# Optimization experiments

Measured on AMD Instinct MI355X. Metric: run time of the kernel, lower is better.

Reference implementation:

```python
import jax, jax.numpy as jnp
import numpy as np

N, B = 128, 8                                # seq_len, batch
V, E, H, S, T = 32000, 256, 256, 256, 32     # vocab, embed, hidden, segment_dim, segment_threshold


def _gru_cell(x, h, Wi, Wh, bi, bh):
    # PyTorch GRU cell convention (gates ordered r,z,n)
    gi = x @ Wi.T + bi
    gh = h @ Wh.T + bh
    ir, iz, inn = jnp.split(gi, 3, axis=-1)
    hr, hz, hn = jnp.split(gh, 3, axis=-1)
    r = jax.nn.sigmoid(ir + hr)
    z = jax.nn.sigmoid(iz + hz)
    n = jnp.tanh(inn + r * hn)
    return (1.0 - z) * n + z * h


def _run_gru(xs, h0, Wi, Wh, bi, bh):
    def step(h, x):
        h = _gru_cell(x, h, Wi, Wh, bi, bh)
        return h, h
    hT, ys = jax.lax.scan(step, h0, xs)
    return ys, hT


def setup_inputs() -> dict:
    key = jax.random.key(0)
    ks = jax.random.split(key, 17)
    sc = 1.0 / np.sqrt(H).astype(np.float32)
    w = lambda k, shape: jax.random.normal(k, shape, jnp.float32) * sc
    return {
        "tokens": jax.random.randint(ks[0], (N, B), 0, V, dtype=jnp.int32),
        "emb": w(ks[1], (V, E)),
        "Wi_f": w(ks[2], (3 * H, E)), "Wh_f": w(ks[3], (3 * H, H)),
        "bi_f": w(ks[4], (3 * H,)),  "bh_f": w(ks[5], (3 * H,)),
        "Wi_r": w(ks[6], (3 * H, E)), "Wh_r": w(ks[7], (3 * H, H)),
        "bi_r": w(ks[8], (3 * H,)),  "bh_r": w(ks[9], (3 * H,)),
        "Wi_s": w(ks[10], (3 * S, 2 * H)), "Wh_s": w(ks[11], (3 * S, S)),
        "bi_s": w(ks[12], (3 * S,)), "bh_s": w(ks[13], (3 * S,)),
        # deterministic stand-ins for the per-start torch.randn initial hiddens
        "h0f": jax.random.normal(ks[14], (N, B, S), jnp.float32),
        "h0b": jax.random.normal(ks[15], (N, B, S), jnp.float32),
    }


def reference(tokens, emb, Wi_f, Wh_f, bi_f, bh_f, Wi_r, Wh_r, bi_r, bh_r,
              Wi_s, Wh_s, bi_s, bh_s, h0f, h0b):
    x = emb[tokens]                                   # (N,B,E); dropout p=0
    h0 = jnp.zeros((B, H), x.dtype)
    ys_f, _ = _run_gru(x, h0, Wi_f, Wh_f, bi_f, bh_f)
    ys_r, _ = _run_gru(x[::-1], h0, Wi_r, Wh_r, bi_r, bh_r)
    outputs = jnp.concatenate([ys_f, ys_r[::-1]], axis=-1)   # (N,B,2H)

    def seg(window, h0i):                             # window (T,B,2H)
        def step(h, xt):
            h = _gru_cell(xt, h, Wi_s, Wh_s, bi_s, bh_s)
            return h, h
        hT, ys = jax.lax.scan(step, h0i, window)
        return ys, hT

    ii = jnp.arange(N)[:, None]                       # (N,1) segment start i
    tt = jnp.arange(T)[None, :]                       # (1,T) step within window
    jf = ii + tt                                      # forward target column j
    jb = ii - tt                                      # backward target row j
    win_f = outputs[jnp.clip(jf, 0, N - 1)]           # (N,T,B,2H)
    win_b = outputs[jnp.clip(jb, 0, N - 1)]
    outs_f, _ = jax.vmap(seg)(win_f, h0f)             # (N,T,B,S)
    outs_b, hT_b = jax.vmap(seg)(win_b, h0b)

    jf_s = jnp.where(jf < N, jf, N)                   # OOB index -> dropped
    jb_s = jnp.where(jb >= 0, jb, N)
    dp_f = jnp.zeros((N, N, B, S), outputs.dtype).at[ii, jf_s].set(outs_f, mode="drop")
    dp_b = jnp.zeros((N, N, B, S), outputs.dtype).at[jb_s, ii].set(outs_b, mode="drop")
    dp = jnp.concatenate([dp_f, dp_b], axis=-1)       # (N,N,B,2S)
    rows, cols = jnp.triu_indices(N)
    dp_tri = dp[rows, cols]                           # (N*(N+1)/2, B, 2S)

    # final hiddens as the torch loops leave them: forward i=N-1 runs exactly
    # one step; backward i=N-1 runs T steps (N >= T so all in range).
    hid_f = _gru_cell(outputs[-1], h0f[-1], Wi_s, Wh_s, bi_s, bh_s)
    hidden = jnp.concatenate([hid_f, hT_b[-1]], axis=-1)[None]  # (1,B,2S)
    return dp_tri, hidden
```

## Files before the change

kernel.cpp:

```cpp
#include <hip/hip_runtime.h>
#include <cstdint>
#include <cstddef>

#define NN 128
#define BB 8
#define EE 256
#define HH 256
#define SS 256
#define TT 32
#define G3 768
#define HBSTR 264
#define HIDOFF 33816576ull
#define OUT_ELEMS 33820672ull

typedef __attribute__((ext_vector_type(8))) short bf16x8;
typedef __attribute__((ext_vector_type(4))) float f32x4;
typedef _Float16 f16;
typedef __attribute__((ext_vector_type(2))) _Float16 f16x2;

__device__ __forceinline__ float bf2f(unsigned short u) {
    union { unsigned u; float f; } v; v.u = ((unsigned)u) << 16; return v.f;
}
__device__ __forceinline__ unsigned short f2bf(float f) {
    union { float f; unsigned u; } v; v.f = f;
    unsigned r = v.u + 0x7fffu + ((v.u >> 16) & 1u);
    return (unsigned short)(r >> 16);
}
__device__ __forceinline__ unsigned short f2h(float f) {
    union { f16 h; unsigned short u; } v; v.h = (f16)f; return v.u;
}
__device__ __forceinline__ float dot2h(unsigned wu, unsigned hu, float acc) {
    union { unsigned u; f16x2 h; } a, b2;
    a.u = wu; b2.u = hu;
    return __builtin_amdgcn_fdot2(a.h, b2.h, acc, false);
}
__device__ __forceinline__ float rcpf(float x) { return __builtin_amdgcn_rcpf(x); }
__device__ __forceinline__ float sigm(float x) { return rcpf(1.f + __expf(-x)); }
__device__ __forceinline__ float tanh_fast(float x) {
    float xc = fminf(fmaxf(x, -10.f), 10.f);
    float e2 = __expf(2.f * xc);
    return (e2 - 1.f) * rcpf(e2 + 1.f);
}

__device__ __forceinline__ int detect_f32(const void* emb) {
    const unsigned* w = (const unsigned*)emb;
    int bad = 0;
    for (int i = 0; i < 128; ++i) {
        unsigned u = w[i];
        bad |= (((u >> 7)  & 0xFFu) >= 0xC8u);
        bad |= (((u >> 23) & 0xFFu) >= 0xC8u);
    }
    return bad;
}
__device__ __forceinline__ float lds1(const void* p, size_t i, int f32) {
    return f32 ? ((const float*)p)[i] : bf2f(((const unsigned short*)p)[i]);
}
__device__ __forceinline__ void outw(void* p, size_t i, float v, int f32) {
    if (f32) ((float*)p)[i] = v;
    else ((unsigned short*)p)[i] = f2bf(v);
}

__global__ __launch_bounds__(256) void conv_all(
    const void* __restrict__ Wi_f, const void* __restrict__ Wi_r,
    const void* __restrict__ Wh_f, const void* __restrict__ Wh_r,
    const void* __restrict__ Wh_s, const void* __restrict__ Wi_s,
    unsigned short* __restrict__ dst, const void* __restrict__ emb) {
    const int f32 = detect_f32(emb);
    size_t i = ((size_t)blockIdx.x * 256 + threadIdx.x) * 8;
    const void* src; size_t off; int h16 = 0;
    if      (i < 196608)  { src = Wi_f; off = i; }
    else if (i < 393216)  { src = Wi_r; off = i - 196608; }
    else if (i < 589824)  { src = Wh_f; off = i - 393216; h16 = 1; }
    else if (i < 786432)  { src = Wh_r; off = i - 589824; h16 = 1; }
    else if (i < 983040)  { src = Wh_s; off = i - 786432; }
    else                  { src = Wi_s; off = i - 983040; }
    bf16x8 v;
    if (f32) {
        const float* q = (const float*)src + off;
        float4 a = *(const float4*)q, b4 = *(const float4*)(q + 4);
        float f[8] = {a.x, a.y, a.z, a.w, b4.x, b4.y, b4.z, b4.w};
#pragma unroll
        for (int j = 0; j < 8; ++j)
            v[j] = (short)(h16 ? f2h(f[j]) : f2bf(f[j]));
    } else {
        v = *(const bf16x8*)((const unsigned short*)src + off);
        if (h16) {
#pragma unroll
            for (int j = 0; j < 8; ++j)
                v[j] = (short)f2h(bf2f((unsigned short)v[j]));
        }
    }
    *(bf16x8*)(dst + i) = v;
}

template <int KK>
__global__ __launch_bounds__(256) void gemm_mfma(
    const int* __restrict__ tok, const void* __restrict__ Asrc,
    const unsigned short* __restrict__ W,  const void* __restrict__ bias,
    unsigned short* __restrict__ C,
    const unsigned short* __restrict__ W2, const void* __restrict__ bias2,
    unsigned short* __restrict__ C2, const void* __restrict__ emb) {

    const int f32 = detect_f32(emb);
    __shared__ unsigned short As[64 * 260];

    int bid = blockIdx.x;
    const unsigned short* Wp = W; const void* bp = bias; unsigned short* Cp = C;
    if (C2 && bid >= 128) { bid -= 128; Wp = W2; bp = bias2; Cp = C2; }
    const int mb = bid >> 3, nb = bid & 7;

    const int tid = threadIdx.x, wave = tid >> 6, lane = tid & 63;
    const int l15 = lane & 15, quad = lane >> 4;

    f32x4 acc[6];
#pragma unroll
    for (int nt = 0; nt < 6; ++nt) acc[nt] = (f32x4){0.f, 0.f, 0.f, 0.f};

    for (int kh = 0; kh < KK; kh += 256) {
        __syncthreads();
        for (int e = tid * 4; e < 64 * 256; e += 1024) {
            int r = e >> 8, k = e & 255;
            int gr = mb * 64 + r;
            unsigned short h4[4];
            if (tok) {
                size_t arow = (size_t)tok[gr] * EE + kh + k;
                if (f32) {
                    float4 v = *(const float4*)((const float*)Asrc + arow);
                    h4[0] = f2bf(v.x); h4[1] = f2bf(v.y); h4[2] = f2bf(v.z); h4[3] = f2bf(v.w);
                } else {
                    *(uint2*)h4 = *(const uint2*)((const unsigned short*)Asrc + arow);
                }
            } else {
                *(uint2*)h4 = *(const uint2*)((const unsigned short*)Asrc + (size_t)gr * KK + kh + k);
            }
            *(uint2*)(As + r * 260 + k) = *(uint2*)h4;
        }
        __syncthreads();
#pragma unroll
        for (int kt = 0; kt < 8; ++kt) {
            bf16x8 Af = *(const bf16x8*)(As + (wave * 16 + l15) * 260 + kt * 32 + quad * 8);
#pragma unroll
            for (int nt = 0; nt < 6; ++nt) {
                int col = nb * 96 + nt * 16 + l15;
                bf16x8 Bfr = *(const bf16x8*)(Wp + (size_t)col * KK + kh + kt * 32 + quad * 8);
                acc[nt] = __builtin_amdgcn_mfma_f32_16x16x32_bf16(Af, Bfr, acc[nt], 0, 0, 0);
            }
        }
    }
#pragma unroll
    for (int nt = 0; nt < 6; ++nt) {
        int col = nb * 96 + nt * 16 + l15;
        float bv = lds1(bp, col, f32);
#pragma unroll
        for (int r4 = 0; r4 < 4; ++r4) {
            int row = mb * 64 + wave * 16 + quad * 4 + r4;
            Cp[(size_t)row * G3 + col] = f2bf(acc[nt][r4] + bv);
        }
    }
}

__global__ __attribute__((amdgpu_flat_work_group_size(512, 512), amdgpu_waves_per_eu(2, 2)))
void token_scan_zero(
    const unsigned short* __restrict__ gi_f, const unsigned short* __restrict__ gi_r,
    const unsigned short* __restrict__ Wh_fh, const unsigned short* __restrict__ Wh_rh,
    const void* __restrict__ bh_f, const void* __restrict__ bh_r,
    unsigned short* __restrict__ outp, void* __restrict__ dout,
    const void* __restrict__ emb) {

    const int f32 = detect_f32(emb);

    if (blockIdx.x >= 16) {
        uint4 z = {0u, 0u, 0u, 0u};
        uint4* p = (uint4*)dout;
        const size_t nvec = OUT_ELEMS * (f32 ? 4 : 2) / 16;
        size_t stride = (size_t)(gridDim.x - 16) * 512;
        for (size_t v = (size_t)(blockIdx.x - 16) * 512 + threadIdx.x; v < nvec; v += stride)
            p[v] = z;
        return;
    }

    const int dir = blockIdx.x & 1;
    const int b   = blockIdx.x >> 1;
    const int tid = threadIdx.x;
    const int c = tid & 255, kh = tid >> 8;

    __shared__ __align__(16) unsigned short hbs[256];
    __shared__ float pr[3][256];

    const unsigned short* Wh = dir ? Wh_rh : Wh_fh;
    const unsigned short* gi = dir ? gi_r : gi_f;
    const void* bh = dir ? bh_r : bh_f;

    unsigned w[192];
#pragma unroll
    for (int g = 0; g < 3; ++g) {
        const unsigned* wp = (const unsigned*)(Wh + (size_t)(g * 256 + c) * 256 + kh * 128);
#pragma unroll
        for (int q = 0; q < 16; ++q) {
            uint4 v = *(const uint4*)(wp + q * 4);
            w[g * 64 + q * 4 + 0] = v.x; w[g * 64 + q * 4 + 1] = v.y;
            w[g * 64 + q * 4 + 2] = v.z; w[g * 64 + q * 4 + 3] = v.w;
        }
    }
#pragma unroll
    for (int i = 0; i < 192; ++i) asm volatile("" : "+v"(w[i]));

    const float bh0 = lds1(bh, c, f32);
    const float bh1 = lds1(bh, c + 256, f32);
    const float bh2 = lds1(bh, c + 512, f32);

    if (tid < 256) hbs[tid] = 0;
    float hreg = 0.f;
    __syncthreads();

    const unsigned* hbw = (const unsigned*)hbs + kh * 64;
    for (int t = 0; t < NN; ++t) {
        const int row = dir ? (NN - 1 - t) : t;
        unsigned short g0 = 0, g1 = 0, g2 = 0;
        if (kh == 0) {
            const unsigned short* gp = gi + (size_t)row * BB * G3 + (size_t)b * G3;
            g0 = gp[c]; g1 = gp[c + 256]; g2 = gp[c + 512];
        }
        float a0 = 0.f, a1 = 0.f, a2 = 0.f;
#pragma unroll
        for (int q = 0; q < 16; ++q) {
            uint4 hv = *(const uint4*)(hbw + q * 4);
            a0 = dot2h(w[      q * 4 + 0], hv.x, a0);
            a0 = dot2h(w[      q * 4 + 1], hv.y, a0);
            a0 = dot2h(w[      q * 4 + 2], hv.z, a0);
            a0 = dot2h(w[      q * 4 + 3], hv.w, a0);
            a1 = dot2h(w[ 64 + q * 4 + 0], hv.x, a1);
            a1 = dot2h(w[ 64 + q * 4 + 1], hv.y, a1);
            a1 = dot2h(w[ 64 + q * 4 + 2], hv.z, a1);
            a1 = dot2h(w[ 64 + q * 4 + 3], hv.w, a1);
            a2 = dot2h(w[128 + q * 4 + 0], hv.x, a2);
            a2 = dot2h(w[128 + q * 4 + 1], hv.y, a2);
            a2 = dot2h(w[128 + q * 4 + 2], hv.z, a2);
            a2 = dot2h(w[128 + q * 4 + 3], hv.w, a2);
        }
        if (kh) { pr[0][c] = a0; pr[1][c] = a1; pr[2][c] = a2; }
        __syncthreads();
        if (kh == 0) {
            a0 += pr[0][c]; a1 += pr[1][c]; a2 += pr[2][c];
            float rr = sigm(bf2f(g0) + a0 + bh0);
            float zz = sigm(bf2f(g1) + a1 + bh1);
            float nn = tanh_fast(bf2f(g2) + rr * (a2 + bh2));
            float hn = (1.f - zz) * nn + zz * hreg;
            hreg = hn;
            hbs[c] = f2h(hn);
        }
        __syncthreads();
        if (kh == 0)
            outp[((size_t)(row * BB + b)) * 512 + dir * 256 + c] = f2bf(hreg);
    }
}

__global__ __attribute__((amdgpu_flat_work_group_size(512, 512), amdgpu_waves_per_eu(2, 2)))
void seg_scan(
    const unsigned short* __restrict__ gi,
    const unsigned short* __restrict__ Whc,
    const void* __restrict__ bh,
    const void* __restrict__ h0f, const void* __restrict__ h0b,
    void* __restrict__ dout, const void* __restrict__ emb) {

    const int f32 = detect_f32(emb);

    __shared__ float gh[BB][G3];
    __shared__ __align__(16) unsigned short hb[16 * HBSTR];

    const int tid = threadIdx.x;
    const int wave = tid >> 6, lane = tid & 63;
    const int l15 = lane & 15, quad = lane >> 4;
    const int dir = blockIdx.x & 1, i0 = blockIdx.x >> 1;

    bf16x8 Ba[8][6];
#pragma unroll
    for (int nt = 0; nt < 6; ++nt) {
        int col = wave * 96 + nt * 16 + l15;
#pragma unroll
        for (int kt = 0; kt < 8; ++kt)
            Ba[kt][nt] = *(const bf16x8*)(Whc + (size_t)col * 256 + kt * 32 + quad * 8);
    }
#pragma unroll
    for (int kt = 0; kt < 8; ++kt)
#pragma unroll
        for (int nt = 0; nt < 6; ++nt) asm volatile("" : "+a"(Ba[kt][nt]));

    const void* h0 = dir ? h0b : h0f;
    const size_t h0base = (size_t)i0 * (BB * SS);
    const int c = tid & 255;
    const int half = tid >> 8;
    const float bh0 = lds1(bh, c, f32);
    const float bh1 = lds1(bh, c + 256, f32);
    const float bh2 = lds1(bh, c + 512, f32);
    float hreg[4];
#pragma unroll
    for (int q = 0; q < 4; ++q) {
        int b = half * 4 + q;
        float v = lds1(h0, h0base + b * 256 + c, f32);
        hreg[q] = v;
        hb[b * HBSTR + c] = f2bf(v);
    }
    for (int e = 8 * HBSTR + tid; e < 16 * HBSTR; e += 512) hb[e] = 0;
    __syncthreads();

    const int nsteps = dir ? min(TT, i0 + 1) : min(TT, NN - i0);
    for (int t = 0; t < nsteps; ++t) {
        const int j = dir ? (i0 - t) : (i0 + t);
        unsigned short gpre[4][3];
        const unsigned short* gp = gi + (size_t)j * BB * G3;
#pragma unroll
        for (int q = 0; q < 4; ++q) {
            int b = half * 4 + q;
            gpre[q][0] = gp[b * G3 + c];
            gpre[q][1] = gp[b * G3 + c + 256];
            gpre[q][2] = gp[b * G3 + c + 512];
        }
        {
            f32x4 acc[6];
#pragma unroll
            for (int nt = 0; nt < 6; ++nt) acc[nt] = (f32x4){0.f, 0.f, 0.f, 0.f};
#pragma unroll
            for (int kt = 0; kt < 8; ++kt) {
                bf16x8 Af = *(const bf16x8*)(hb + l15 * HBSTR + kt * 32 + quad * 8);
#pragma unroll
                for (int nt = 0; nt < 6; ++nt)
                    acc[nt] = __builtin_amdgcn_mfma_f32_16x16x32_bf16(Af, Ba[kt][nt], acc[nt], 0, 0, 0);
            }
            if (quad < 2) {
#pragma unroll
                for (int nt = 0; nt < 6; ++nt) {
                    int col = wave * 96 + nt * 16 + l15;
#pragma unroll
                    for (int r4 = 0; r4 < 4; ++r4) gh[quad * 4 + r4][col] = acc[nt][r4];
                }
            }
        }
        __syncthreads();

#pragma unroll
        for (int q = 0; q < 4; ++q) {
            int b = half * 4 + q;
            float rr = sigm(bf2f(gpre[q][0]) + gh[b][c] + bh0);
            float zz = sigm(bf2f(gpre[q][1]) + gh[b][c + 256] + bh1);
            float nn = tanh_fast(bf2f(gpre[q][2]) + rr * (gh[b][c + 512] + bh2));
            float hn = (1.f - zz) * nn + zz * hreg[q];
            hreg[q] = hn;
            hb[b * HBSTR + c] = f2bf(hn);
        }
        __syncthreads();

        const int r0 = dir ? j : i0;
        const size_t tri = (size_t)r0 * NN - (size_t)(r0 * (r0 - 1)) / 2 + t;
        const size_t obase = tri * (BB * 512) + (dir ? 256 : 0);
#pragma unroll
        for (int q = 0; q < 4; ++q) {
            int b = half * 4 + q;
            outw(dout, obase + b * 512 + c, hreg[q], f32);
            if (i0 == NN - 1) {
                if (dir == 0 && t == 0)      outw(dout, HIDOFF + b * 512 + c, hreg[q], f32);
                if (dir == 1 && t == TT - 1) outw(dout, HIDOFF + 256 + b * 512 + c, hreg[q], f32);
            }
        }
    }
}

extern "C" void kernel_launch(void* const* d_in, const int* in_sizes, int n_in,
                              void* d_out, int out_size, void* d_ws, size_t ws_size,
                              hipStream_t stream) {
    const int* tokens = (const int*)d_in[0];
    const void* emb   = d_in[1];
    const void* Wi_f  = d_in[2];
    const void* Wh_f  = d_in[3];
    const void* bi_f  = d_in[4];
    const void* bh_f  = d_in[5];
    const void* Wi_r  = d_in[6];
    const void* Wh_r  = d_in[7];
    const void* bi_r  = d_in[8];
    const void* bh_r  = d_in[9];
    const void* Wi_s  = d_in[10];
    const void* Wh_s  = d_in[11];
    const void* bi_s  = d_in[12];
    const void* bh_s  = d_in[13];
    const void* h0f   = d_in[14];
    const void* h0b   = d_in[15];

    unsigned short* wsu = (unsigned short*)d_ws;
    unsigned short* gif  = wsu;
    unsigned short* gir  = wsu + 786432;
    unsigned short* outp = wsu + 1572864;
    unsigned short* wcv  = wsu + 2097152;
    unsigned short* gis  = gif;

    const unsigned short* Wi_fc = wcv;
    const unsigned short* Wi_rc = wcv + 196608;
    const unsigned short* Wh_fh = wcv + 393216;
    const unsigned short* Wh_rh = wcv + 589824;
    const unsigned short* Wh_sc = wcv + 786432;
    const unsigned short* Wi_sc = wcv + 983040;

    conv_all<<<dim3(672), dim3(256), 0, stream>>>(Wi_f, Wi_r, Wh_f, Wh_r, Wh_s, Wi_s,
                                                  wcv, emb);
    gemm_mfma<256><<<dim3(256), dim3(256), 0, stream>>>(
        tokens, emb, Wi_fc, bi_f, gif, Wi_rc, bi_r, gir, emb);
    token_scan_zero<<<dim3(256), dim3(512), 0, stream>>>(gif, gir, Wh_fh, Wh_rh,
                                                         bh_f, bh_r, outp, d_out, emb);
    gemm_mfma<512><<<dim3(128), dim3(256), 0, stream>>>(
        nullptr, outp, Wi_sc, bi_s, gis, nullptr, nullptr, nullptr, emb);
    seg_scan<<<dim3(256), dim3(512), 0, stream>>>(gis, Wh_sc, bh_s, h0f, h0b, d_out, emb);
}
```

Baseline: 539.0 us.

## Halve seg_scan block to 4 waves holding 12 weight tiles each; nontemporal zero stores

seg_scan now runs with 256 threads (4 waves) instead of 512. Each wave keeps 12 MFMA column tiles of the recurrent weight, split between AGPRs and VGPRs, and each thread handles all 8 batch elements in the elementwise GRU update. This raises per-wave MFMA work but halves the waves that synchronize at each barrier, and it targets one wave per EU, so latency hiding is lower and register pressure is high. Separately, the output-zeroing loop uses nontemporal stores to avoid polluting the cache.

```diff
diff --git a/kernel.cpp b/kernel.cpp
--- a/kernel.cpp
+++ b/kernel.cpp
@@ -15,6 +15,7 @@
 
 typedef __attribute__((ext_vector_type(8))) short bf16x8;
 typedef __attribute__((ext_vector_type(4))) float f32x4;
+typedef __attribute__((ext_vector_type(4))) unsigned u32x4;
 typedef _Float16 f16;
 typedef __attribute__((ext_vector_type(2))) _Float16 f16x2;
 
@@ -170,12 +171,12 @@
     const int f32 = detect_f32(emb);
 
     if (blockIdx.x >= 16) {
-        uint4 z = {0u, 0u, 0u, 0u};
-        uint4* p = (uint4*)dout;
+        u32x4 z = (u32x4){0u, 0u, 0u, 0u};
+        u32x4* p = (u32x4*)dout;
         const size_t nvec = OUT_ELEMS * (f32 ? 4 : 2) / 16;
         size_t stride = (size_t)(gridDim.x - 16) * 512;
         for (size_t v = (size_t)(blockIdx.x - 16) * 512 + threadIdx.x; v < nvec; v += stride)
-            p[v] = z;
+            __builtin_nontemporal_store(z, p + v);
         return;
     }
 
@@ -255,7 +256,7 @@
     }
 }
 
-__global__ __attribute__((amdgpu_flat_work_group_size(512, 512), amdgpu_waves_per_eu(2, 2)))
+__global__ __attribute__((amdgpu_flat_work_group_size(256, 256), amdgpu_waves_per_eu(1, 1)))
 void seg_scan(
     const unsigned short* __restrict__ gi,
     const unsigned short* __restrict__ Whc,
@@ -273,64 +274,69 @@
     const int l15 = lane & 15, quad = lane >> 4;
     const int dir = blockIdx.x & 1, i0 = blockIdx.x >> 1;
 
-    bf16x8 Ba[8][6];
-#pragma unroll
-    for (int nt = 0; nt < 6; ++nt) {
-        int col = wave * 96 + nt * 16 + l15;
-#pragma unroll
-        for (int kt = 0; kt < 8; ++kt)
-            Ba[kt][nt] = *(const bf16x8*)(Whc + (size_t)col * 256 + kt * 32 + quad * 8);
-    }
-#pragma unroll
-    for (int kt = 0; kt < 8; ++kt)
-#pragma unroll
-        for (int nt = 0; nt < 6; ++nt) asm volatile("" : "+a"(Ba[kt][nt]));
+    bf16x8 Ba[8][8]; bf16x8 Bv[8][4];
+#pragma unroll
+    for (int nt = 0; nt < 12; ++nt) {
+        int col = wave * 192 + nt * 16 + l15;
+#pragma unroll
+        for (int kt = 0; kt < 8; ++kt) {
+            bf16x8 f = *(const bf16x8*)(Whc + (size_t)col * 256 + kt * 32 + quad * 8);
+            if (nt < 8) Ba[kt][nt] = f; else Bv[kt][nt - 8] = f;
+        }
+    }
+#pragma unroll
+    for (int kt = 0; kt < 8; ++kt) {
+#pragma unroll
+        for (int nt = 0; nt < 8; ++nt) asm volatile("" : "+a"(Ba[kt][nt]));
+#pragma unroll
+        for (int nt = 0; nt < 4; ++nt) asm volatile("" : "+v"(Bv[kt][nt]));
+    }
 
     const void* h0 = dir ? h0b : h0f;
     const size_t h0base = (size_t)i0 * (BB * SS);
-    const int c = tid & 255;
-    const int half = tid >> 8;
+    const int c = tid;
     const float bh0 = lds1(bh, c, f32);
     const float bh1 = lds1(bh, c + 256, f32);
     const float bh2 = lds1(bh, c + 512, f32);
-    float hreg[4];
-#pragma unroll
-    for (int q = 0; q < 4; ++q) {
-        int b = half * 4 + q;
+    float hreg[BB];
+#pragma unroll
+    for (int b = 0; b < BB; ++b) {
         float v = lds1(h0, h0base + b * 256 + c, f32);
-        hreg[q] = v;
+        hreg[b] = v;
         hb[b * HBSTR + c] = f2bf(v);
     }
-    for (int e = 8 * HBSTR + tid; e < 16 * HBSTR; e += 512) hb[e] = 0;
+    for (int e = 8 * HBSTR + tid; e < 16 * HBSTR; e += 256) hb[e] = 0;
     __syncthreads();
 
     const int nsteps = dir ? min(TT, i0 + 1) : min(TT, NN - i0);
     for (int t = 0; t < nsteps; ++t) {
         const int j = dir ? (i0 - t) : (i0 + t);
-        unsigned short gpre[4][3];
+        unsigned short gpre[BB][3];
         const unsigned short* gp = gi + (size_t)j * BB * G3;
 #pragma unroll
-        for (int q = 0; q < 4; ++q) {
-            int b = half * 4 + q;
-            gpre[q][0] = gp[b * G3 + c];
-            gpre[q][1] = gp[b * G3 + c + 256];
-            gpre[q][2] = gp[b * G3 + c + 512];
+        for (int b = 0; b < BB; ++b) {
+            gpre[b][0] = gp[b * G3 + c];
+            gpre[b][1] = gp[b * G3 + c + 256];
+            gpre[b][2] = gp[b * G3 + c + 512];
         }
         {
-            f32x4 acc[6];
-#pragma unroll
-            for (int nt = 0; nt < 6; ++nt) acc[nt] = (f32x4){0.f, 0.f, 0.f, 0.f};
+            f32x4 acc[12];
+#pragma unroll
+            for (int nt = 0; nt < 12; ++nt) acc[nt] = (f32x4){0.f, 0.f, 0.f, 0.f};
 #pragma unroll
             for (int kt = 0; kt < 8; ++kt) {
                 bf16x8 Af = *(const bf16x8*)(hb + l15 * HBSTR + kt * 32 + quad * 8);
 #pragma unroll
-                for (int nt = 0; nt < 6; ++nt)
+                for (int nt = 0; nt < 8; ++nt)
                     acc[nt] = __builtin_amdgcn_mfma_f32_16x16x32_bf16(Af, Ba[kt][nt], acc[nt], 0, 0, 0);
+#pragma unroll
+                for (int nt = 0; nt < 4; ++nt)
+                    acc[8 + nt] = __builtin_amdgcn_mfma_f32_16x16x32_bf16(Af, Bv[kt][nt], acc[8 + nt], 0, 0, 0);
             }
             if (quad < 2) {
 #pragma unroll
-                for (int nt = 0; nt < 6; ++nt) {
-                    int col = wave * 96 + nt * 16 + l15;
+                for (int nt = 0; nt < 12; ++nt) {
+                    int col = wave * 192 + nt * 16 + l15;
 #pragma unroll
                     for (int r4 = 0; r4 < 4; ++r4) gh[quad * 4 + r4][col] = acc[nt][r4];
                 }
@@ -339,13 +345,12 @@
         __syncthreads();
 
 #pragma unroll
-        for (int q = 0; q < 4; ++q) {
-            int b = half * 4 + q;
-            float rr = sigm(bf2f(gpre[q][0]) + gh[b][c] + bh0);
-            float zz = sigm(bf2f(gpre[q][1]) + gh[b][c + 256] + bh1);
-            float nn = tanh_fast(bf2f(gpre[q][2]) + rr * (gh[b][c + 512] + bh2));
-            float hn = (1.f - zz) * nn + zz * hreg[q];
-            hreg[q] = hn;
+        for (int b = 0; b < BB; ++b) {
+            float rr = sigm(bf2f(gpre[b][0]) + gh[b][c] + bh0);
+            float zz = sigm(bf2f(gpre[b][1]) + gh[b][c + 256] + bh1);
+            float nn = tanh_fast(bf2f(gpre[b][2]) + rr * (gh[b][c + 512] + bh2));
+            float hn = (1.f - zz) * nn + zz * hreg[b];
+            hreg[b] = hn;
             hb[b * HBSTR + c] = f2bf(hn);
         }
         __syncthreads();
@@ -354,12 +359,11 @@
         const size_t tri = (size_t)r0 * NN - (size_t)(r0 * (r0 - 1)) / 2 + t;
         const size_t obase = tri * (BB * 512) + (dir ? 256 : 0);
 #pragma unroll
-        for (int q = 0; q < 4; ++q) {
-            int b = half * 4 + q;
-            outw(dout, obase + b * 512 + c, hreg[q], f32);
+        for (int b = 0; b < BB; ++b) {
+            outw(dout, obase + b * 512 + c, hreg[b], f32);
             if (i0 == NN - 1) {
-                if (dir == 0 && t == 0)      outw(dout, HIDOFF + b * 512 + c, hreg[q], f32);
-                if (dir == 1 && t == TT - 1) outw(dout, HIDOFF + 256 + b * 512 + c, hreg[q], f32);
+                if (dir == 0 && t == 0)      outw(dout, HIDOFF + b * 512 + c, hreg[b], f32);
+                if (dir == 1 && t == TT - 1) outw(dout, HIDOFF + 256 + b * 512 + c, hreg[b], f32);
             }
         }
     }
@@ -407,5 +411,5 @@
                                                          bh_f, bh_r, outp, d_out, emb);
     gemm_mfma<512><<<dim3(128), dim3(256), 0, stream>>>(
         nullptr, outp, Wi_sc, bi_s, gis, nullptr, nullptr, nullptr, emb);
-    seg_scan<<<dim3(256), dim3(512), 0, stream>>>(gis, Wh_sc, bh_s, h0f, h0b, d_out, emb);
-}
+    seg_scan<<<dim3(256), dim3(256), 0, stream>>>(gis, Wh_sc, bh_s, h0f, h0b, d_out, emb);
+}
```

New measurement: 505.9 us. 6.1% less time.
